# Kernel tuning notes

Hardware: AMD Instinct MI355X
Metric: run time of the kernel (lower is better)

## Reference

```python
import jax, jax.numpy as jnp
import numpy as np

H, D = 20, 64  # heads, head_dim (hidden_size = 1280)


def setup_inputs() -> dict:
    key = jax.random.key(0)
    ks = jax.random.split(key, 10)
    B, S, HID, CROSS, T_TXT, T_IP = 8, 4096, 1280, 2048, 77, 4
    w = lambda k, shp: jax.random.normal(k, shp, dtype=jnp.float32) * 0.02
    return {
        "hidden_states": jax.random.normal(ks[0], (B, S, HID), dtype=jnp.float32),
        "encoder_hidden_states": jax.random.normal(ks[1], (B, T_TXT, CROSS), dtype=jnp.float32),
        "ip_hidden_states": jax.random.normal(ks[2], (B, T_IP, CROSS), dtype=jnp.float32),
        "Wq": w(ks[3], (HID, HID)),
        "Wk": w(ks[4], (CROSS, HID)),
        "Wv": w(ks[5], (CROSS, HID)),
        "Wk_ip": w(ks[6], (CROSS, HID)),
        "Wv_ip": w(ks[7], (CROSS, HID)),
        "Wo": w(ks[8], (HID, HID)),
        "bo": jnp.zeros((HID,), dtype=jnp.float32),
    }


def _attend(q, kv_in, Wk, Wv):
    # q: [B,S,H,D]; kv_in: [B,T,cross]
    B, T = kv_in.shape[0], kv_in.shape[1]
    k = (kv_in @ Wk).reshape(B, T, H, D)
    v = (kv_in @ Wv).reshape(B, T, H, D)
    scale = 1.0 / jnp.sqrt(jnp.asarray(D, q.dtype))
    scores = jnp.einsum("bqhd,bkhd->bhqk", q, k) * scale
    probs = jax.nn.softmax(scores, axis=-1)
    out = jnp.einsum("bhqk,bkhd->bqhd", probs, v)
    return out.reshape(B, q.shape[1], H * D)


def reference(hidden_states, encoder_hidden_states, ip_hidden_states,
              Wq, Wk, Wv, Wk_ip, Wv_ip, Wo, bo):
    B, S, _ = hidden_states.shape
    q = (hidden_states @ Wq).reshape(B, S, H, D)
    # text cross-attention branch
    out = _attend(q, encoder_hidden_states, Wk, Wv)
    # IP-adapter branch (single adapter, scale=1.0, no mask)
    ip_scale = 1.0
    out = out + ip_scale * _attend(q, ip_hidden_states, Wk_ip, Wv_ip)
    # output projection (dropout is identity at inference)
    return out @ Wo + bo
```

## Files before the change

kernel.cpp:

```cpp
#include <hip/hip_runtime.h>

using u16 = unsigned short;
using u32 = unsigned int;
typedef __bf16 bf16x8 __attribute__((ext_vector_type(8)));
typedef float f32x4 __attribute__((ext_vector_type(4)));
typedef float f32x16 __attribute__((ext_vector_type(16)));

__device__ __forceinline__ u16 f2bf(float f) {
  u32 u = __float_as_uint(f);
  u += 0x7FFFu + ((u >> 16) & 1u);
  return (u16)(u >> 16);
}

__device__ __forceinline__ u32 cvtpk(float a, float b) {
  u32 r;
  asm("v_cvt_pk_bf16_f32 %0, %1, %2" : "=v"(r) : "v"(a), "v"(b));
  return r;
}

__device__ __forceinline__ void gload16(const u16* g, u16* l) {
  __builtin_amdgcn_global_load_lds((const __attribute__((address_space(1))) void*)g,
                                   (__attribute__((address_space(3))) void*)l, 16, 0, 0);
}

__global__ void f32_to_bf16_vec(const float* __restrict__ in, u16* __restrict__ out, long n4) {
  const long i = (long)blockIdx.x * 256 + threadIdx.x;
  if (i >= n4) return;
  const float4 v = ((const float4*)in)[i];
  ushort4 o;
  o.x = f2bf(v.x); o.y = f2bf(v.y); o.z = f2bf(v.z); o.w = f2bf(v.w);
  ((ushort4*)out)[i] = o;
}

__global__ void build_a_all(const float* __restrict__ enc, const float* __restrict__ ip,
                            u16* __restrict__ out) {
  const int i = blockIdx.x * 256 + threadIdx.x;
  const int row = i >> 9;
  const int c4 = i & 511;
  ushort4 o = {0, 0, 0, 0};
  const float4* src = nullptr;
  if (row < 616) src = (const float4*)enc + (size_t)row * 512 + c4;
  else if (row >= 640 && row < 672) src = (const float4*)ip + (size_t)(row - 640) * 512 + c4;
  if (src) {
    const float4 v = *src;
    o.x = f2bf(v.x); o.y = f2bf(v.y); o.z = f2bf(v.z); o.w = f2bf(v.w);
  }
  ((ushort4*)out)[i] = o;
}

__global__ void transpose_w4(const float* __restrict__ s0, const float* __restrict__ s1,
                             const float* __restrict__ s2, const float* __restrict__ s3,
                             u16* __restrict__ dst) {
  __shared__ float tile[32][33];
  const int z = blockIdx.z;
  const float* in = (z == 0) ? s0 : (z == 1) ? s1 : (z == 2) ? s2 : s3;
  u16* out = dst + (size_t)z * 1280 * 2048;
  const int K = 2048, N = 1280;
  const int n0 = blockIdx.x << 5, k0 = blockIdx.y << 5;
  const int x = threadIdx.x, y = threadIdx.y;
#pragma unroll
  for (int i = 0; i < 32; i += 8)
    tile[y + i][x] = in[(size_t)(k0 + y + i) * N + n0 + x];
  __syncthreads();
#pragma unroll
  for (int i = 0; i < 32; i += 8)
    out[(size_t)(n0 + y + i) * K + k0 + x] = f2bf(tile[x][y + i]);
}

__global__ void transpose_w2(const float* __restrict__ s0, const float* __restrict__ s1,
                             u16* __restrict__ d0, u16* __restrict__ d1) {
  __shared__ float tile[32][33];
  const int z = blockIdx.z;
  const float* in = z ? s1 : s0;
  u16* out = z ? d1 : d0;
  const int K = 1280, N = 1280;
  const int n0 = blockIdx.x << 5, k0 = blockIdx.y << 5;
  const int x = threadIdx.x, y = threadIdx.y;
#pragma unroll
  for (int i = 0; i < 32; i += 8)
    tile[y + i][x] = in[(size_t)(k0 + y + i) * N + n0 + x];
  __syncthreads();
#pragma unroll
  for (int i = 0; i < 32; i += 8)
    out[(size_t)(n0 + y + i) * K + k0 + x] = f2bf(tile[x][y + i]);
}

#define MFMA16(a, b, c) __builtin_amdgcn_mfma_f32_16x16x32_bf16(a, b, c, 0, 0, 0)
#define MFMA32(a, b, c) __builtin_amdgcn_mfma_f32_32x32x16_bf16(a, b, c, 0, 0, 0)

template <int F32OUT>
__global__ __launch_bounds__(512, 2) void gemm256(
    const u16* __restrict__ A, const u16* __restrict__ Bt,
    u16* __restrict__ Cb, float* __restrict__ Cf, const float* __restrict__ bias,
    int M, int N, int K) {
  __shared__ __align__(16) u16 smem[65536];
  u16* As = smem;
  u16* Bs = smem + 32768;

  const int tid = threadIdx.x;
  const int w = tid >> 6, lane = tid & 63;
  const int lo = lane & 15, hi = lane >> 4;
  const int wm = w >> 2, wn = w & 3;

  const int nbn = N >> 8;
  int wg = blockIdx.x;
  {
    const int nwg = gridDim.x;
    const int q = nwg >> 3, r = nwg & 7;
    const int xcd = wg & 7, l = wg >> 3;
    wg = (xcd < r ? xcd * (q + 1) : r * (q + 1) + (xcd - r) * q) + l;
  }
  const int bm = wg / nbn, bn = wg % nbn;
  const int m0 = bm << 8, n0 = bn << 8;
  const int NT = K >> 6;

  const int sr = lane >> 3;
  const int sc8 = ((lane & 7) ^ sr) << 3;
  const u16* pA[2];
  const u16* pB[2];
#pragma unroll
  for (int i = 0; i < 2; ++i) {
    const int rr = (i * 8 + w) * 8 + sr;
    pA[i] = A + (size_t)(m0 + rr) * K + sc8;
    pB[i] = Bt + (size_t)(n0 + rr) * K + sc8;
  }
  const int ch0 = w * 512, ch1 = (8 + w) * 512;

#define STAGE_A(h, tt)                                                     \
  {                                                                        \
    const int ttc = ((tt) < NT) ? (tt) : (NT - 1);                         \
    u16* d = As + ((((tt)&1) * 2 + (h)) << 13);                            \
    const size_t off = (size_t)(h)*128 * K + (size_t)ttc * 64;             \
    gload16(pA[0] + off, d + ch0);                                         \
    gload16(pA[1] + off, d + ch1);                                         \
  }
#define STAGE_B(h, tt)                                                     \
  {                                                                        \
    const int ttc = ((tt) < NT) ? (tt) : (NT - 1);                         \
    u16* d = Bs + ((((tt)&1) * 2 + (h)) << 13);                            \
    const size_t off = (size_t)(h)*128 * K + (size_t)ttc * 64;             \
    gload16(pB[0] + off, d + ch0);                                         \
    gload16(pB[1] + off, d + ch1);                                         \
  }

  const int low0 = (lo << 7) | ((hi ^ (lo & 7)) << 4);
  const int low1 = (lo << 7) | (((4 | hi) ^ (lo & 7)) << 4);

  f32x4 acc[8][4];
#pragma unroll
  for (int i = 0; i < 8; ++i)
#pragma unroll
    for (int j = 0; j < 4; ++j) acc[i][j] = (f32x4){0.f, 0.f, 0.f, 0.f};

  STAGE_B(0, 0); STAGE_B(1, 0);
  STAGE_A(0, 0); STAGE_A(1, 0);
  STAGE_B(0, 1); STAGE_B(1, 1);

  const char* aSm = (const char*)As;
  const char* bSm = (const char*)Bs;

  for (int t = 0; t < NT; ++t) {
    const int p = t & 1;
    const int aBase = (p * 2 + wm) << 14;
    const int bBase = ((p * 2 + (wn >> 1)) << 14) + ((wn & 1) << 13);

    asm volatile("s_waitcnt vmcnt(4)" ::: "memory");
    asm volatile("s_barrier" ::: "memory");

    bf16x8 a0[4][2], a1[4][2], b0[2][2], b1[2][2];
#pragma unroll
    for (int mf = 0; mf < 4; ++mf) {
      a0[mf][0] = *(const bf16x8*)(aSm + aBase + (mf << 11) + low0);
      a0[mf][1] = *(const bf16x8*)(aSm + aBase + (mf << 11) + low1);
    }
#pragma unroll
    for (int nf = 0; nf < 2; ++nf) {
      b0[nf][0] = *(const bf16x8*)(bSm + bBase + (nf << 11) + low0);
      b0[nf][1] = *(const bf16x8*)(bSm + bBase + (nf << 11) + low1);
    }
    STAGE_A(0, t + 1);
    __builtin_amdgcn_s_setprio(1);
#pragma unroll
    for (int mf = 0; mf < 4; ++mf)
#pragma unroll
      for (int nf = 0; nf < 2; ++nf) {
        acc[mf][nf] = MFMA16(a0[mf][0], b0[nf][0], acc[mf][nf]);
        acc[mf][nf] = MFMA16(a0[mf][1], b0[nf][1], acc[mf][nf]);
      }
    __builtin_amdgcn_s_setprio(0);
    asm volatile("s_barrier" ::: "memory");

#pragma unroll
    for (int nf = 0; nf < 2; ++nf) {
      b1[nf][0] = *(const bf16x8*)(bSm + bBase + (1 << 12) + (nf << 11) + low0);
      b1[nf][1] = *(const bf16x8*)(bSm + bBase + (1 << 12) + (nf << 11) + low1);
    }
    STAGE_A(1, t + 1);
    __builtin_amdgcn_s_setprio(1);
#pragma unroll
    for (int mf = 0; mf < 4; ++mf)
#pragma unroll
      for (int nf = 0; nf < 2; ++nf) {
        acc[mf][2 + nf] = MFMA16(a0[mf][0], b1[nf][0], acc[mf][2 + nf]);
        acc[mf][2 + nf] = MFMA16(a0[mf][1], b1[nf][1], acc[mf][2 + nf]);
      }
    __builtin_amdgcn_s_setprio(0);
    asm volatile("s_barrier" ::: "memory");

#pragma unroll
    for (int mf = 0; mf < 4; ++mf) {
      a1[mf][0] = *(const bf16x8*)(aSm + aBase + (1 << 13) + (mf << 11) + low0);
      a1[mf][1] = *(const bf16x8*)(aSm + aBase + (1 << 13) + (mf << 11) + low1);
    }
    STAGE_B(0, t + 2);
    __builtin_amdgcn_s_setprio(1);
#pragma unroll
    for (int mf = 0; mf < 4; ++mf)
#pragma unroll
      for (int nf = 0; nf < 2; ++nf) {
        acc[4 + mf][nf] = MFMA16(a1[mf][0], b0[nf][0], acc[4 + mf][nf]);
        acc[4 + mf][nf] = MFMA16(a1[mf][1], b0[nf][1], acc[4 + mf][nf]);
      }
    __builtin_amdgcn_s_setprio(0);
    asm volatile("s_barrier" ::: "memory");

    STAGE_B(1, t + 2);
    __builtin_amdgcn_s_setprio(1);
#pragma unroll
    for (int mf = 0; mf < 4; ++mf)
#pragma unroll
      for (int nf = 0; nf < 2; ++nf) {
        acc[4 + mf][2 + nf] = MFMA16(a1[mf][0], b1[nf][0], acc[4 + mf][2 + nf]);
        acc[4 + mf][2 + nf] = MFMA16(a1[mf][1], b1[nf][1], acc[4 + mf][2 + nf]);
      }
    __builtin_amdgcn_s_setprio(0);
  }

#pragma unroll
  for (int g = 0; g < 2; ++g)
#pragma unroll
    for (int mf = 0; mf < 4; ++mf)
#pragma unroll
      for (int ng = 0; ng < 2; ++ng)
#pragma unroll
        for (int nfi = 0; nfi < 2; ++nfi) {
          const f32x4 v = acc[g * 4 + mf][ng * 2 + nfi];
          const int row0 = m0 + wm * 128 + g * 64 + mf * 16 + hi * 4;
          const int col = n0 + wn * 64 + ng * 32 + nfi * 16 + lo;
          if (F32OUT) {
            const float bb = bias[col];
#pragma unroll
            for (int r = 0; r < 4; ++r)
              Cf[(size_t)(row0 + r) * N + col] = v[r] + bb;
          } else {
#pragma unroll
            for (int r = 0; r < 4; ++r)
              Cb[(size_t)(row0 + r) * N + col] = f2bf(v[r]);
          }
        }
#undef STAGE_A
#undef STAGE_B
}

__global__ __launch_bounds__(256) void build_vt(const u16* __restrict__ kvc,
                                                u16* __restrict__ vt) {
  __shared__ u16 Ls[96][72];
  const int tid = threadIdx.x;
  const int h = blockIdx.x % 20, b = blockIdx.x / 20;
  for (int idx = tid; idx < 96 * 8; idx += 256) {
    const int row = idx >> 3, c8 = (idx & 7) << 3;
    uint4 val = make_uint4(0, 0, 0, 0);
    if (row < 77)
      val = *(const uint4*)(kvc + (size_t)(b * 77 + row) * 5120 + 1280 + h * 64 + c8);
    else if (row >= 80 && row < 84)
      val = *(const uint4*)(kvc + (size_t)(640 + b * 4 + row - 80) * 5120 + 3840 + h * 64 + c8);
    *(uint4*)&Ls[row][c8] = val;
  }
  __syncthreads();
  u16* dst = vt + (size_t)blockIdx.x * 64 * 96;
  for (int idx = tid; idx < 768; idx += 256) {
    const int d = idx / 12, c = (idx % 12) * 8;
    u16 tmp[8];
#pragma unroll
    for (int j = 0; j < 8; ++j) tmp[j] = Ls[c + j][d];
    *(uint4*)(dst + d * 96 + c) = *(const uint4*)tmp;
  }
}

__global__ __launch_bounds__(256) void attn3(
    const u16* __restrict__ Q, const u16* __restrict__ kvc,
    const u16* __restrict__ vt, u16* __restrict__ O) {
  const int tid = threadIdx.x;
  const int w = tid >> 6, lane = tid & 63;
  const int l31 = lane & 31, hi5 = lane >> 5;
  const int bid = blockIdx.x;
  const int qc = bid & 15;
  const int h = (bid >> 4) % 20;
  const int b = bid / 320;
  const int q0 = qc * 256 + w * 64;
  const size_t qbase = (size_t)b * 4096 + q0;

  bf16x8 qf0[4], qf1[4];
  {
    const u16* qp0 = Q + (qbase + l31) * 1280 + h * 64 + hi5 * 8;
    const u16* qp1 = Q + (qbase + 32 + l31) * 1280 + h * 64 + hi5 * 8;
#pragma unroll
    for (int dc = 0; dc < 4; ++dc) {
      qf0[dc] = *(const bf16x8*)(qp0 + dc * 16);
      qf1[dc] = *(const bf16x8*)(qp1 + dc * 16);
    }
  }

  f32x16 s0[3], s1[3];
#pragma unroll
  for (int kf = 0; kf < 3; ++kf)
#pragma unroll
    for (int r = 0; r < 16; ++r) { s0[kf][r] = 0.f; s1[kf][r] = 0.f; }

#pragma unroll
  for (int kf = 0; kf < 3; ++kf) {
    const int key = kf * 32 + l31;
    const u16* kp;
    if (key < 77) kp = kvc + (size_t)(b * 77 + key) * 5120 + h * 64 + hi5 * 8;
    else if (key >= 80 && key < 84)
      kp = kvc + (size_t)(640 + b * 4 + key - 80) * 5120 + 2560 + h * 64 + hi5 * 8;
    else kp = kvc + h * 64 + hi5 * 8;
    bf16x8 ka[4];
#pragma unroll
    for (int dc = 0; dc < 4; ++dc) ka[dc] = *(const bf16x8*)(kp + dc * 16);
#pragma unroll
    for (int dc = 0; dc < 4; ++dc) {
      s0[kf] = MFMA32(ka[dc], qf0[dc], s0[kf]);
      s1[kf] = MFMA32(ka[dc], qf1[dc], s1[kf]);
    }
  }

  float st0 = 0.f, si0 = 0.f, st1 = 0.f, si1 = 0.f;
#pragma unroll
  for (int kf = 0; kf < 3; ++kf)
#pragma unroll
    for (int r = 0; r < 16; ++r) {
      const int krem = (r & 3) + 8 * (r >> 2);
      const int k = kf * 32 + krem + 4 * hi5;
      const bool vtx = k < 77;
      const bool vip = (k >= 80) & (k < 84);
      const float e0 = (vtx | vip) ? __expf(s0[kf][r] * 0.125f) : 0.f;
      const float e1 = (vtx | vip) ? __expf(s1[kf][r] * 0.125f) : 0.f;
      s0[kf][r] = e0; s1[kf][r] = e1;
      st0 += vtx ? e0 : 0.f; si0 += vip ? e0 : 0.f;
      st1 += vtx ? e1 : 0.f; si1 += vip ? e1 : 0.f;
    }
  st0 += __shfl_xor(st0, 32); si0 += __shfl_xor(si0, 32);
  st1 += __shfl_xor(st1, 32); si1 += __shfl_xor(si1, 32);
  const float rt0 = __fdividef(1.f, st0), ri0 = __fdividef(1.f, si0);
  const float rt1 = __fdividef(1.f, st1), ri1 = __fdividef(1.f, si1);
#pragma unroll
  for (int kf = 0; kf < 3; ++kf)
#pragma unroll
    for (int r = 0; r < 16; ++r) {
      const int krem = (r & 3) + 8 * (r >> 2);
      const int k = kf * 32 + krem + 4 * hi5;
      const bool vip = (k >= 80) & (k < 84);
      s0[kf][r] *= vip ? ri0 : rt0;
      s1[kf][r] *= vip ? ri1 : rt1;
    }

  const u16* vbase = vt + ((size_t)(b * 20 + h) * 64) * 96 + hi5 * 8;

#define PV_STORE(sA, qoff)                                                  \
  {                                                                         \
    f32x16 acc[2];                                                          \
    _Pragma("unroll") for (int nf = 0; nf < 2; ++nf)                        \
    _Pragma("unroll") for (int r = 0; r < 16; ++r) acc[nf][r] = 0.f;        \
    _Pragma("unroll") for (int ks = 0; ks < 6; ++ks) {                      \
      const int kf = ks >> 1;                                               \
      const int rb = (ks & 1) * 8;                                          \
      const u32 lo01 = cvtpk(sA[kf][rb + 0], sA[kf][rb + 1]);               \
      const u32 lo23 = cvtpk(sA[kf][rb + 2], sA[kf][rb + 3]);               \
      const u32 hi01 = cvtpk(sA[kf][rb + 4], sA[kf][rb + 5]);               \
      const u32 hi23 = cvtpk(sA[kf][rb + 6], sA[kf][rb + 7]);               \
      const u32 plo01 = __shfl_xor(lo01, 32);                               \
      const u32 plo23 = __shfl_xor(lo23, 32);                               \
      const u32 phi01 = __shfl_xor(hi01, 32);                               \
      const u32 phi23 = __shfl_xor(hi23, 32);                               \
      union { u32 u[4]; bf16x8 v; } pu;                                     \
      pu.u[0] = hi5 ? phi01 : lo01;                                         \
      pu.u[1] = hi5 ? phi23 : lo23;                                         \
      pu.u[2] = hi5 ? hi01 : plo01;                                         \
      pu.u[3] = hi5 ? hi23 : plo23;                                         \
      _Pragma("unroll") for (int nf = 0; nf < 2; ++nf) {                    \
        const bf16x8 vb =                                                   \
            *(const bf16x8*)(vbase + (size_t)(nf * 32 + l31) * 96 + ks * 16);\
        acc[nf] = MFMA32(pu.v, vb, acc[nf]);                                \
      }                                                                     \
    }                                                                       \
    _Pragma("unroll") for (int nf = 0; nf < 2; ++nf)                        \
    _Pragma("unroll") for (int r = 0; r < 16; ++r) {                        \
      const int row = q0 + (qoff) + (r & 3) + 8 * (r >> 2) + 4 * hi5;       \
      O[((size_t)b * 4096 + row) * 1280 + h * 64 + nf * 32 + l31] =         \
          f2bf(acc[nf][r]);                                                 \
    }                                                                       \
  }

  PV_STORE(s0, 0)
  PV_STORE(s1, 32)
#undef PV_STORE
}

extern "C" void kernel_launch(void* const* d_in, const int* in_sizes, int n_in,
                              void* d_out, int out_size, void* d_ws, size_t ws_size,
                              hipStream_t stream) {
  (void)in_sizes; (void)n_in; (void)out_size; (void)ws_size;
  const float* hs   = (const float*)d_in[0];
  const float* enc  = (const float*)d_in[1];
  const float* ip   = (const float*)d_in[2];
  const float* Wq   = (const float*)d_in[3];
  const float* Wk   = (const float*)d_in[4];
  const float* Wv   = (const float*)d_in[5];
  const float* Wkip = (const float*)d_in[6];
  const float* Wvip = (const float*)d_in[7];
  const float* Wo   = (const float*)d_in[8];
  const float* bo   = (const float*)d_in[9];
  float* out = (float*)d_out;

  u16* q_bf  = (u16*)d_out;
  u16* hs_bf = (u16*)d_out + 41943040;

  char* ws = (char*)d_ws;
  u16* kvc   = (u16*)(ws);
  u16* wo_t  = (u16*)(ws + 15728640);
  u16* vt    = (u16*)(ws + 19005440);
  u16* attn  = (u16*)(ws + 20971520);
  u16* wq_t  = attn;
  u16* kvw   = (u16*)(ws + 20971520 + 3276800);
  u16* a_all = (u16*)(ws + 20971520 + 24248320);

  f32_to_bf16_vec<<<40960, 256, 0, stream>>>(hs, hs_bf, 10485760);
  build_a_all<<<1536, 256, 0, stream>>>(enc, ip, a_all);

  dim3 tb(32, 8);
  transpose_w4<<<dim3(40, 64, 4), tb, 0, stream>>>(Wk, Wv, Wkip, Wvip, kvw);
  transpose_w2<<<dim3(40, 40, 2), tb, 0, stream>>>(Wq, Wo, wq_t, wo_t);

  gemm256<0><<<640, 512, 0, stream>>>(hs_bf, wq_t, q_bf, nullptr, nullptr, 32768, 1280, 1280);
  gemm256<0><<<60, 512, 0, stream>>>(a_all, kvw, kvc, nullptr, nullptr, 768, 5120, 2048);

  build_vt<<<160, 256, 0, stream>>>(kvc, vt);

  attn3<<<2560, 256, 0, stream>>>(q_bf, kvc, vt, attn);

  gemm256<1><<<640, 512, 0, stream>>>(attn, wo_t, nullptr, out, bo, 32768, 1280, 1280);
}
```

Baseline: 408.2 us.

## Fuse cross-attention into the Q projection GEMM epilogue

The Q projection GEMM now stages each warp's 128x64 bf16 Q tile (one head) in LDS, then runs both the text and IP-adapter attention and softmax directly in the epilogue, writing attention output instead of Q. This removes the separate attention kernel launch and the round trip of the 84 MB bf16 Q tensor through HBM. In exchange, the GEMM kernel's epilogue becomes much heavier, with more registers and slightly larger LDS. That may reduce occupancy or spill, and it serialises the attention work behind the GEMM tiles.

```diff
diff --git a/kernel.cpp b/kernel.cpp
--- a/kernel.cpp
+++ b/kernel.cpp
@@ -88,12 +88,13 @@
 #define MFMA16(a, b, c) __builtin_amdgcn_mfma_f32_16x16x32_bf16(a, b, c, 0, 0, 0)
 #define MFMA32(a, b, c) __builtin_amdgcn_mfma_f32_32x32x16_bf16(a, b, c, 0, 0, 0)
 
-template <int F32OUT>
+template <int MODE>
 __global__ __launch_bounds__(512, 2) void gemm256(
     const u16* __restrict__ A, const u16* __restrict__ Bt,
     u16* __restrict__ Cb, float* __restrict__ Cf, const float* __restrict__ bias,
+    const u16* __restrict__ kvcP, const u16* __restrict__ vtP,
     int M, int N, int K) {
-  __shared__ __align__(16) u16 smem[65536];
+  __shared__ __align__(16) u16 smem[67584];
   u16* As = smem;
   u16* Bs = smem + 32768;
 
@@ -236,28 +237,159 @@
     __builtin_amdgcn_s_setprio(0);
   }
 
-#pragma unroll
-  for (int g = 0; g < 2; ++g)
-#pragma unroll
-    for (int mf = 0; mf < 4; ++mf)
-#pragma unroll
-      for (int ng = 0; ng < 2; ++ng)
-#pragma unroll
-        for (int nfi = 0; nfi < 2; ++nfi) {
-          const f32x4 v = acc[g * 4 + mf][ng * 2 + nfi];
-          const int row0 = m0 + wm * 128 + g * 64 + mf * 16 + hi * 4;
-          const int col = n0 + wn * 64 + ng * 32 + nfi * 16 + lo;
-          if (F32OUT) {
-            const float bb = bias[col];
-#pragma unroll
-            for (int r = 0; r < 4; ++r)
-              Cf[(size_t)(row0 + r) * N + col] = v[r] + bb;
-          } else {
-#pragma unroll
-            for (int r = 0; r < 4; ++r)
-              Cb[(size_t)(row0 + r) * N + col] = f2bf(v[r]);
+  if (MODE != 2) {
+#pragma unroll
+    for (int g = 0; g < 2; ++g)
+#pragma unroll
+      for (int mf = 0; mf < 4; ++mf)
+#pragma unroll
+        for (int ng = 0; ng < 2; ++ng)
+#pragma unroll
+          for (int nfi = 0; nfi < 2; ++nfi) {
+            const f32x4 v = acc[g * 4 + mf][ng * 2 + nfi];
+            const int row0 = m0 + wm * 128 + g * 64 + mf * 16 + hi * 4;
+            const int col = n0 + wn * 64 + ng * 32 + nfi * 16 + lo;
+            if (MODE == 1) {
+              const float bb = bias[col];
+#pragma unroll
+              for (int r = 0; r < 4; ++r)
+                Cf[(size_t)(row0 + r) * N + col] = v[r] + bb;
+            } else {
+#pragma unroll
+              for (int r = 0; r < 4; ++r)
+                Cb[(size_t)(row0 + r) * N + col] = f2bf(v[r]);
+            }
           }
+  } else {
+    asm volatile("s_waitcnt vmcnt(0)" ::: "memory");
+    __builtin_amdgcn_s_barrier();
+
+    u16* qlds = smem + w * 8448;
+#pragma unroll
+    for (int g = 0; g < 2; ++g)
+#pragma unroll
+      for (int mf = 0; mf < 4; ++mf)
+#pragma unroll
+        for (int ng = 0; ng < 2; ++ng)
+#pragma unroll
+          for (int nfi = 0; nfi < 2; ++nfi) {
+            const f32x4 v = acc[g * 4 + mf][ng * 2 + nfi];
+            const int qrow = g * 64 + mf * 16 + hi * 4;
+            const int d = ng * 32 + nfi * 16 + lo;
+#pragma unroll
+            for (int r = 0; r < 4; ++r) qlds[(qrow + r) * 66 + d] = f2bf(v[r]);
+          }
+
+    const int l31 = lane & 31, hi5 = lane >> 5;
+    const int h = bn * 4 + wn;
+    const int b = m0 >> 12;
+    const u16* vbase = vtP + ((size_t)(b * 20 + h) * 64) * 96 + hi5 * 8;
+    const int rowB = m0 + wm * 128;
+
+#pragma unroll
+    for (int pass = 0; pass < 2; ++pass) {
+      bf16x8 qf0[4], qf1[4];
+#pragma unroll
+      for (int dc = 0; dc < 4; ++dc) {
+        qf0[dc] = *(const bf16x8*)&qlds[(pass * 64 + l31) * 66 + dc * 16 + hi5 * 8];
+        qf1[dc] = *(const bf16x8*)&qlds[(pass * 64 + 32 + l31) * 66 + dc * 16 + hi5 * 8];
+      }
+
+      f32x16 s0[3], s1[3];
+#pragma unroll
+      for (int kf = 0; kf < 3; ++kf)
+#pragma unroll
+        for (int r = 0; r < 16; ++r) { s0[kf][r] = 0.f; s1[kf][r] = 0.f; }
+
+#pragma unroll
+      for (int kf = 0; kf < 3; ++kf) {
+        const int key = kf * 32 + l31;
+        const u16* kp;
+        if (key < 77) kp = kvcP + (size_t)(b * 77 + key) * 5120 + h * 64 + hi5 * 8;
+        else if (key >= 80 && key < 84)
+          kp = kvcP + (size_t)(640 + b * 4 + key - 80) * 5120 + 2560 + h * 64 + hi5 * 8;
+        else kp = kvcP + h * 64 + hi5 * 8;
+        bf16x8 ka[4];
+#pragma unroll
+        for (int dc = 0; dc < 4; ++dc) ka[dc] = *(const bf16x8*)(kp + dc * 16);
+#pragma unroll
+        for (int dc = 0; dc < 4; ++dc) {
+          s0[kf] = MFMA32(ka[dc], qf0[dc], s0[kf]);
+          s1[kf] = MFMA32(ka[dc], qf1[dc], s1[kf]);
         }
+      }
+
+      float st0 = 0.f, si0 = 0.f, st1 = 0.f, si1 = 0.f;
+#pragma unroll
+      for (int kf = 0; kf < 3; ++kf)
+#pragma unroll
+        for (int r = 0; r < 16; ++r) {
+          const int krem = (r & 3) + 8 * (r >> 2);
+          const int k = kf * 32 + krem + 4 * hi5;
+          const bool vtx = k < 77;
+          const bool vip = (k >= 80) & (k < 84);
+          const float e0 = (vtx | vip) ? __expf(s0[kf][r] * 0.125f) : 0.f;
+          const float e1 = (vtx | vip) ? __expf(s1[kf][r] * 0.125f) : 0.f;
+          s0[kf][r] = e0; s1[kf][r] = e1;
+          st0 += vtx ? e0 : 0.f; si0 += vip ? e0 : 0.f;
+          st1 += vtx ? e1 : 0.f; si1 += vip ? e1 : 0.f;
+        }
+      st0 += __shfl_xor(st0, 32); si0 += __shfl_xor(si0, 32);
+      st1 += __shfl_xor(st1, 32); si1 += __shfl_xor(si1, 32);
+      const float rt0 = __fdividef(1.f, st0), ri0 = __fdividef(1.f, si0);
+      const float rt1 = __fdividef(1.f, st1), ri1 = __fdividef(1.f, si1);
+#pragma unroll
+      for (int kf = 0; kf < 3; ++kf)
+#pragma unroll
+        for (int r = 0; r < 16; ++r) {
+          const int krem = (r & 3) + 8 * (r >> 2);
+          const int k = kf * 32 + krem + 4 * hi5;
+          const bool vip = (k >= 80) & (k < 84);
+          s0[kf][r] *= vip ? ri0 : rt0;
+          s1[kf][r] *= vip ? ri1 : rt1;
+        }
+
+#define PV_STORE(sA, qoff)                                                  \
+      {                                                                     \
+        f32x16 pacc[2];                                                     \
+        _Pragma("unroll") for (int nf = 0; nf < 2; ++nf)                    \
+        _Pragma("unroll") for (int r = 0; r < 16; ++r) pacc[nf][r] = 0.f;   \
+        _Pragma("unroll") for (int ks = 0; ks < 6; ++ks) {                  \
+          const int kf = ks >> 1;                                           \
+          const int rb = (ks & 1) * 8;                                      \
+          const u32 lo01 = cvtpk(sA[kf][rb + 0], sA[kf][rb + 1]);           \
+          const u32 lo23 = cvtpk(sA[kf][rb + 2], sA[kf][rb + 3]);           \
+          const u32 hi01 = cvtpk(sA[kf][rb + 4], sA[kf][rb + 5]);           \
+          const u32 hi23 = cvtpk(sA[kf][rb + 6], sA[kf][rb + 7]);           \
+          const u32 plo01 = __shfl_xor(lo01, 32);                           \
+          const u32 plo23 = __shfl_xor(lo23, 32);                           \
+          const u32 phi01 = __shfl_xor(hi01, 32);                           \
+          const u32 phi23 = __shfl_xor(hi23, 32);                           \
+          union { u32 u[4]; bf16x8 v; } pu;                                 \
+          pu.u[0] = hi5 ? phi01 : lo01;                                     \
+          pu.u[1] = hi5 ? phi23 : lo23;                                     \
+          pu.u[2] = hi5 ? hi01 : plo01;                                     \
+          pu.u[3] = hi5 ? hi23 : plo23;                                     \
+          _Pragma("unroll") for (int nf = 0; nf < 2; ++nf) {                \
+            const bf16x8 vb = *(const bf16x8*)(vbase +                      \
+                (size_t)(nf * 32 + l31) * 96 + ks * 16);                    \
+            pacc[nf] = MFMA32(pu.v, vb, pacc[nf]);                          \
+          }                                                                 \
+        }                                                                   \
+        _Pragma("unroll") for (int nf = 0; nf < 2; ++nf)                    \
+        _Pragma("unroll") for (int r = 0; r < 16; ++r) {                    \
+          const int row = rowB + pass * 64 + (qoff) +                       \
+                          (r & 3) + 8 * (r >> 2) + 4 * hi5;                 \
+          Cb[(size_t)row * 1280 + h * 64 + nf * 32 + l31] =                 \
+              f2bf(pacc[nf][r]);                                            \
+        }                                                                   \
+      }
+
+      PV_STORE(s0, 0)
+      PV_STORE(s1, 32)
+#undef PV_STORE
+    }
+  }
 #undef STAGE_A
 #undef STAGE_B
 }
@@ -285,126 +417,6 @@
     for (int j = 0; j < 8; ++j) tmp[j] = Ls[c + j][d];
     *(uint4*)(dst + d * 96 + c) = *(const uint4*)tmp;
   }
-}
-
-__global__ __launch_bounds__(256) void attn3(
-    const u16* __restrict__ Q, const u16* __restrict__ kvc,
-    const u16* __restrict__ vt, u16* __restrict__ O) {
-  const int tid = threadIdx.x;
-  const int w = tid >> 6, lane = tid & 63;
-  const int l31 = lane & 31, hi5 = lane >> 5;
-  const int bid = blockIdx.x;
-  const int qc = bid & 15;
-  const int h = (bid >> 4) % 20;
-  const int b = bid / 320;
-  const int q0 = qc * 256 + w * 64;
-  const size_t qbase = (size_t)b * 4096 + q0;
-
-  bf16x8 qf0[4], qf1[4];
-  {
-    const u16* qp0 = Q + (qbase + l31) * 1280 + h * 64 + hi5 * 8;
-    const u16* qp1 = Q + (qbase + 32 + l31) * 1280 + h * 64 + hi5 * 8;
-#pragma unroll
-    for (int dc = 0; dc < 4; ++dc) {
-      qf0[dc] = *(const bf16x8*)(qp0 + dc * 16);
-      qf1[dc] = *(const bf16x8*)(qp1 + dc * 16);
-    }
-  }
-
-  f32x16 s0[3], s1[3];
-#pragma unroll
-  for (int kf = 0; kf < 3; ++kf)
-#pragma unroll
-    for (int r = 0; r < 16; ++r) { s0[kf][r] = 0.f; s1[kf][r] = 0.f; }
-
-#pragma unroll
-  for (int kf = 0; kf < 3; ++kf) {
-    const int key = kf * 32 + l31;
-    const u16* kp;
-    if (key < 77) kp = kvc + (size_t)(b * 77 + key) * 5120 + h * 64 + hi5 * 8;
-    else if (key >= 80 && key < 84)
-      kp = kvc + (size_t)(640 + b * 4 + key - 80) * 5120 + 2560 + h * 64 + hi5 * 8;
-    else kp = kvc + h * 64 + hi5 * 8;
-    bf16x8 ka[4];
-#pragma unroll
-    for (int dc = 0; dc < 4; ++dc) ka[dc] = *(const bf16x8*)(kp + dc * 16);
-#pragma unroll
-    for (int dc = 0; dc < 4; ++dc) {
-      s0[kf] = MFMA32(ka[dc], qf0[dc], s0[kf]);
-      s1[kf] = MFMA32(ka[dc], qf1[dc], s1[kf]);
-    }
-  }
-
-  float st0 = 0.f, si0 = 0.f, st1 = 0.f, si1 = 0.f;
-#pragma unroll
-  for (int kf = 0; kf < 3; ++kf)
-#pragma unroll
-    for (int r = 0; r < 16; ++r) {
-      const int krem = (r & 3) + 8 * (r >> 2);
-      const int k = kf * 32 + krem + 4 * hi5;
-      const bool vtx = k < 77;
-      const bool vip = (k >= 80) & (k < 84);
-      const float e0 = (vtx | vip) ? __expf(s0[kf][r] * 0.125f) : 0.f;
-      const float e1 = (vtx | vip) ? __expf(s1[kf][r] * 0.125f) : 0.f;
-      s0[kf][r] = e0; s1[kf][r] = e1;
-      st0 += vtx ? e0 : 0.f; si0 += vip ? e0 : 0.f;
-      st1 += vtx ? e1 : 0.f; si1 += vip ? e1 : 0.f;
-    }
-  st0 += __shfl_xor(st0, 32); si0 += __shfl_xor(si0, 32);
-  st1 += __shfl_xor(st1, 32); si1 += __shfl_xor(si1, 32);
-  const float rt0 = __fdividef(1.f, st0), ri0 = __fdividef(1.f, si0);
-  const float rt1 = __fdividef(1.f, st1), ri1 = __fdividef(1.f, si1);
-#pragma unroll
-  for (int kf = 0; kf < 3; ++kf)
-#pragma unroll
-    for (int r = 0; r < 16; ++r) {
-      const int krem = (r & 3) + 8 * (r >> 2);
-      const int k = kf * 32 + krem + 4 * hi5;
-      const bool vip = (k >= 80) & (k < 84);
-      s0[kf][r] *= vip ? ri0 : rt0;
-      s1[kf][r] *= vip ? ri1 : rt1;
-    }
-
-  const u16* vbase = vt + ((size_t)(b * 20 + h) * 64) * 96 + hi5 * 8;
-
-#define PV_STORE(sA, qoff)                                                  \
-  {                                                                         \
-    f32x16 acc[2];                                                          \
-    _Pragma("unroll") for (int nf = 0; nf < 2; ++nf)                        \
-    _Pragma("unroll") for (int r = 0; r < 16; ++r) acc[nf][r] = 0.f;        \
-    _Pragma("unroll") for (int ks = 0; ks < 6; ++ks) {                      \
-      const int kf = ks >> 1;                                               \
-      const int rb = (ks & 1) * 8;                                          \
-      const u32 lo01 = cvtpk(sA[kf][rb + 0], sA[kf][rb + 1]);               \
-      const u32 lo23 = cvtpk(sA[kf][rb + 2], sA[kf][rb + 3]);               \
-      const u32 hi01 = cvtpk(sA[kf][rb + 4], sA[kf][rb + 5]);               \
-      const u32 hi23 = cvtpk(sA[kf][rb + 6], sA[kf][rb + 7]);               \
-      const u32 plo01 = __shfl_xor(lo01, 32);                               \
-      const u32 plo23 = __shfl_xor(lo23, 32);                               \
-      const u32 phi01 = __shfl_xor(hi01, 32);                               \
-      const u32 phi23 = __shfl_xor(hi23, 32);                               \
-      union { u32 u[4]; bf16x8 v; } pu;                                     \
-      pu.u[0] = hi5 ? phi01 : lo01;                                         \
-      pu.u[1] = hi5 ? phi23 : lo23;                                         \
-      pu.u[2] = hi5 ? hi01 : plo01;                                         \
-      pu.u[3] = hi5 ? hi23 : plo23;                                         \
-      _Pragma("unroll") for (int nf = 0; nf < 2; ++nf) {                    \
-        const bf16x8 vb =                                                   \
-            *(const bf16x8*)(vbase + (size_t)(nf * 32 + l31) * 96 + ks * 16);\
-        acc[nf] = MFMA32(pu.v, vb, acc[nf]);                                \
-      }                                                                     \
-    }                                                                       \
-    _Pragma("unroll") for (int nf = 0; nf < 2; ++nf)                        \
-    _Pragma("unroll") for (int r = 0; r < 16; ++r) {                        \
-      const int row = q0 + (qoff) + (r & 3) + 8 * (r >> 2) + 4 * hi5;       \
-      O[((size_t)b * 4096 + row) * 1280 + h * 64 + nf * 32 + l31] =         \
-          f2bf(acc[nf][r]);                                                 \
-    }                                                                       \
-  }
-
-  PV_STORE(s0, 0)
-  PV_STORE(s1, 32)
-#undef PV_STORE
 }
 
 extern "C" void kernel_launch(void* const* d_in, const int* in_sizes, int n_in,
@@ -423,7 +435,7 @@
   const float* bo   = (const float*)d_in[9];
   float* out = (float*)d_out;
 
-  u16* q_bf  = (u16*)d_out;
+  u16* wq_t  = (u16*)d_out;
   u16* hs_bf = (u16*)d_out + 41943040;
 
   char* ws = (char*)d_ws;
@@ -431,7 +443,6 @@
   u16* wo_t  = (u16*)(ws + 15728640);
   u16* vt    = (u16*)(ws + 19005440);
   u16* attn  = (u16*)(ws + 20971520);
-  u16* wq_t  = attn;
   u16* kvw   = (u16*)(ws + 20971520 + 3276800);
   u16* a_all = (u16*)(ws + 20971520 + 24248320);
 
@@ -442,12 +453,13 @@
   transpose_w4<<<dim3(40, 64, 4), tb, 0, stream>>>(Wk, Wv, Wkip, Wvip, kvw);
   transpose_w2<<<dim3(40, 40, 2), tb, 0, stream>>>(Wq, Wo, wq_t, wo_t);
 
-  gemm256<0><<<640, 512, 0, stream>>>(hs_bf, wq_t, q_bf, nullptr, nullptr, 32768, 1280, 1280);
-  gemm256<0><<<60, 512, 0, stream>>>(a_all, kvw, kvc, nullptr, nullptr, 768, 5120, 2048);
-
+  gemm256<0><<<60, 512, 0, stream>>>(a_all, kvw, kvc, nullptr, nullptr, nullptr, nullptr,
+                                     768, 5120, 2048);
   build_vt<<<160, 256, 0, stream>>>(kvc, vt);
 
-  attn3<<<2560, 256, 0, stream>>>(q_bf, kvc, vt, attn);
-
-  gemm256<1><<<640, 512, 0, stream>>>(attn, wo_t, nullptr, out, bo, 32768, 1280, 1280);
-}
+  gemm256<2><<<640, 512, 0, stream>>>(hs_bf, wq_t, attn, nullptr, nullptr, kvc, vt,
+                                      32768, 1280, 1280);
+
+  gemm256<1><<<640, 512, 0, stream>>>(attn, wo_t, nullptr, out, bo, nullptr, nullptr,
+                                      32768, 1280, 1280);
+}
```

Result: faster. 373.4 us (-8.5%).
